# Kernel optimization log

Hardware: AMD Instinct MI355X
Metric: run time of the kernel (lower is better)

## Reference

```python
import jax, jax.numpy as jnp
import numpy as np
from jax import lax

N_ITERS = 3
NUM_CAPS_IN = 768   # 32 * 4 * 6
NUM_CAPS_OUT = 64
CAPS_DIM_IN = 8
CAPS_DIM_OUT = 16


def _conv2d(x, w, b, stride):
    # x: NCHW, w: OIHW, VALID padding
    y = lax.conv_general_dilated(x, w, (stride, stride), 'VALID',
                                 dimension_numbers=('NCHW', 'OIHW', 'NCHW'))
    return y + b[None, :, None, None]


def _squash(x, axis):
    # norm**2 / (1 + norm**2) * x / norm  (as in the torch source)
    norm = jnp.linalg.norm(x, axis=axis, keepdims=True)
    return (norm ** 2) / (1.0 + norm ** 2) * x / norm


def setup_inputs() -> dict:
    key = jax.random.key(0)
    ks = jax.random.split(key, 4)
    B = 128
    x = jax.random.normal(ks[0], (B, 3, 32, 42), dtype=jnp.float32)
    conv1_w = jax.random.normal(ks[1], (32, 3, 6, 6), dtype=jnp.float32) * 0.1
    conv1_b = jnp.zeros((32,), dtype=jnp.float32)
    pc_w = jax.random.normal(ks[2], (256, 32, 3, 3), dtype=jnp.float32) * 0.1
    pc_b = jnp.zeros((256,), dtype=jnp.float32)
    # FinalCapsule W: (num_caps_in, num_caps_out, caps_dim_out, caps_dim_in)
    route_w = jax.random.normal(ks[3], (NUM_CAPS_IN, NUM_CAPS_OUT, CAPS_DIM_OUT, CAPS_DIM_IN), dtype=jnp.float32)
    return {"x": x, "conv1_w": conv1_w, "conv1_b": conv1_b,
            "pc_w": pc_w, "pc_b": pc_b, "route_w": route_w}


def reference(x, conv1_w, conv1_b, pc_w, pc_b, route_w):
    B = x.shape[0]
    # conv1: k=6, s=3 -> (B,32,9,13)
    h = jax.nn.relu(_conv2d(x, conv1_w, conv1_b, 3))
    # primary capsules: k=3, s=2 -> (B,256,4,6) -> (B,768,8)
    h = _conv2d(h, pc_w, pc_b, 2)
    u = h.reshape(B, -1, CAPS_DIM_IN)
    u = _squash(u, axis=-1)
    # prediction vectors: W[i,o,:,:] @ u[b,i,:] -> xh (B, 768, 64, 16)
    xh = jnp.einsum('iokd,bid->biok', route_w, u)
    xhd = lax.stop_gradient(xh)
    b_logits = jnp.zeros((B, NUM_CAPS_IN, NUM_CAPS_OUT), dtype=xh.dtype)
    for _ in range(N_ITERS - 1):
        c = jax.nn.softmax(b_logits, axis=2)                      # (B,768,64)
        s = jnp.sum(c[..., None] * xhd, axis=1, keepdims=True)   # (B,1,64,16)
        v = _squash(s, axis=-1)
        b_logits = b_logits + jnp.sum(xhd * v, axis=-1)
    c = jax.nn.softmax(b_logits, axis=2)
    s = jnp.sum(c[..., None] * xh, axis=1, keepdims=True)
    v = _squash(s, axis=-1)                                       # (B,1,64,16)
    return v[:, 0].reshape(B, NUM_CAPS_OUT * CAPS_DIM_OUT)        # (B,1024)
```

## Files before the change

### kernel.cpp

```cpp
#include <hip/hip_runtime.h>
#include <math.h>

#define BATCH 128
#define NCI 768
#define NCO 64
#define DIN 8
#define DOUT 16

typedef __attribute__((ext_vector_type(8))) short bfrag;
typedef __attribute__((ext_vector_type(4))) float f32x4;
typedef __attribute__((ext_vector_type(16))) float f32x16;

__device__ __forceinline__ void split8(const float* x, bfrag& hi, bfrag& lo) {
    #pragma unroll
    for (int j = 0; j < 8; ++j) {
        unsigned xb = __float_as_uint(x[j]);
        unsigned hb = xb & 0xffff0000u;
        float lf = x[j] - __uint_as_float(hb);
        hi[j] = (short)(xb >> 16);
        lo[j] = (short)(__float_as_uint(lf) >> 16);
    }
}

__global__ __launch_bounds__(256) void conv1_kernel(
    const float* __restrict__ x, const float* __restrict__ w,
    const float* __restrict__ bias, float* __restrict__ h1) {
    __shared__ float wl[32 * 3 * 36];
    for (int i = threadIdx.x; i < 3456; i += 256) wl[i] = w[i];
    __syncthreads();
    int idx = blockIdx.x * 256 + threadIdx.x;
    const int total = BATCH * 32 * 9 * 13;
    if (idx >= total) return;
    int ow = idx % 13; int t = idx / 13;
    int oh = t % 9; t /= 9;
    int oc = t % 32; int b = t / 32;
    float acc = bias[oc];
    const float* xb = x + (size_t)b * 3 * 32 * 42;
    #pragma unroll
    for (int ic = 0; ic < 3; ++ic) {
        const float* xc = xb + ic * 32 * 42 + (oh * 3) * 42 + ow * 3;
        const float* wc = wl + (oc * 3 + ic) * 36;
        #pragma unroll
        for (int kh = 0; kh < 6; ++kh)
            #pragma unroll
            for (int kw = 0; kw < 6; ++kw)
                acc += xc[kh * 42 + kw] * wc[kh * 6 + kw];
    }
    h1[idx] = fmaxf(acc, 0.f);
}

__global__ __launch_bounds__(256) void im2col_kernel(
    const float* __restrict__ h1, float* __restrict__ B2) {
    int idx = blockIdx.x * 256 + threadIdx.x;
    if (idx >= 36 * 3072) return;
    int n = idx % 3072, ko = idx / 3072;
    int b = n / 24, s = n % 24, h = s / 6, w = s % 6;
    const float* hb = h1 + (size_t)b * 3744 + (2 * h) * 13 + 2 * w;
    float out[8];
    #pragma unroll
    for (int j = 0; j < 8; ++j) {
        int k = ko * 8 + j;
        int ic = k / 9, r = k % 9;
        int kh = r / 3, kw = r % 3;
        out[j] = hb[ic * 117 + kh * 13 + kw];
    }
    *(float4*)(B2 + (size_t)idx * 8) = *(const float4*)out;
    *(float4*)(B2 + (size_t)idx * 8 + 4) = *(const float4*)(out + 4);
}

__global__ __launch_bounds__(256) void pc_gemm_kernel(
    const float* __restrict__ wpc, const float* __restrict__ bias,
    const float* __restrict__ B2, float* __restrict__ u2) {
    int wv = threadIdx.x >> 6;
    int l = threadIdx.x & 63;
    int q = l >> 4, r16 = l & 15;
    int c2t = blockIdx.y * 4 + wv;
    int n0 = blockIdx.x * 16;
    f32x4 acc = {0.f, 0.f, 0.f, 0.f};
    int c2a = c2t * 16 + r16;
    const float* ap0 = wpc + (size_t)c2a * 288 + q * 8;
    const float* bp0 = B2 + ((size_t)q * 3072 + n0 + r16) * 8;
    #pragma unroll
    for (int ks = 0; ks < 9; ++ks) {
        float av[8], bv[8];
        *(float4*)av = *(const float4*)(ap0 + ks * 32);
        *(float4*)(av + 4) = *(const float4*)(ap0 + ks * 32 + 4);
        *(float4*)bv = *(const float4*)(bp0 + (size_t)ks * 4 * 3072 * 8);
        *(float4*)(bv + 4) = *(const float4*)(bp0 + (size_t)ks * 4 * 3072 * 8 + 4);
        bfrag ahi, alo, bhi, blo;
        split8(av, ahi, alo);
        split8(bv, bhi, blo);
        acc = __builtin_amdgcn_mfma_f32_16x16x32_bf16(ahi, bhi, acc, 0, 0, 0);
        acc = __builtin_amdgcn_mfma_f32_16x16x32_bf16(ahi, blo, acc, 0, 0, 0);
        acc = __builtin_amdgcn_mfma_f32_16x16x32_bf16(alo, bhi, acc, 0, 0, 0);
    }
    int n = n0 + r16;
    int b = n / 24, s = n % 24;
    float vals[4], n2[4];
    #pragma unroll
    for (int r = 0; r < 4; ++r) {
        float xv = acc[r] + bias[c2t * 16 + q * 4 + r];
        vals[r] = xv;
        n2[r] = xv * xv;
    }
    #pragma unroll
    for (int r = 0; r < 4; ++r) {
        n2[r] += __shfl_xor(n2[r], 1, 64);
        n2[r] += __shfl_xor(n2[r], 2, 64);
        n2[r] += __shfl_xor(n2[r], 4, 64);
    }
    #pragma unroll
    for (int r = 0; r < 4; ++r) {
        int c2 = c2t * 16 + q * 4 + r;
        int cap = c2 * 3 + (s >> 3);
        int d = s & 7;
        float nr = sqrtf(n2[r]);
        u2[((size_t)(cap * 2 + (d >> 2)) * 128 + b) * 4 + (d & 3)]
            = vals[r] * nr / (1.f + n2[r]);
    }
}

__global__ __launch_bounds__(128) void mz_kernel(
    const float* __restrict__ blog, float* __restrict__ m_, float* __restrict__ z_) {
    int i = blockIdx.x;
    int b = threadIdx.x;
    const float* src = blog + (size_t)i * 128 + b;
    float r[64];
    float m = -1e30f;
    #pragma unroll
    for (int o = 0; o < 64; ++o) {
        r[o] = src[(size_t)o * 98304];
        m = fmaxf(m, r[o]);
    }
    float sum = 0.f;
    #pragma unroll
    for (int o = 0; o < 64; ++o) sum += __expf(r[o] - m);
    m_[i * 128 + b] = m;
    z_[i * 128 + b] = 1.f / sum;
}

template <bool UNIFORM>
__global__ __launch_bounds__(256, 4) void spass_kernel(
    const float* __restrict__ W, const float* __restrict__ u2,
    const float* __restrict__ blog, const float* __restrict__ m_,
    const float* __restrict__ z_, float* __restrict__ s_part) {
    int o = blockIdx.x;
    int it = blockIdx.y;
    int tid = threadIdx.x;
    int wv = tid >> 6;
    int l = tid & 63;
    int q = l >> 4, r16 = l & 15;
    int i0 = it * 32;
    __shared__ float wl[32 * 132];

    float4 ua[3][2][2];
    float bl[3][2], mv[3][2], zv[3][2];
    auto issue = [&](int s, int buf) {
        int cap = i0 + s * 4 + q;
        #pragma unroll
        for (int m = 0; m < 2; ++m) {
            int b = wv * 32 + m * 16 + r16;
            ua[buf][m][0] = *(const float4*)(u2 + ((size_t)(cap * 2 + 0) * 128 + b) * 4);
            ua[buf][m][1] = *(const float4*)(u2 + ((size_t)(cap * 2 + 1) * 128 + b) * 4);
            if (!UNIFORM) {
                bl[buf][m] = blog[((size_t)o * 768 + cap) * 128 + b];
                mv[buf][m] = m_[cap * 128 + b];
                zv[buf][m] = z_[cap * 128 + b];
            }
        }
    };

    issue(0, 0);
    issue(1, 1);
    #pragma unroll
    for (int itr = 0; itr < 4; ++itr) {
        int F = tid + 256 * itr;
        int cap = F >> 5, slot = F & 31;
        float4 t4 = *(const float4*)(W + ((size_t)(i0 + cap) * 64 + o) * 128 + slot * 4);
        *(float4*)(wl + cap * 132 + slot * 4) = t4;
    }
    __syncthreads();

    f32x4 acc0 = {0.f, 0.f, 0.f, 0.f};
    f32x4 acc1 = {0.f, 0.f, 0.f, 0.f};
    #pragma unroll
    for (int s = 0; s < 8; ++s) {
        int cur = s % 3;
        if (s < 6) issue(s + 2, (s + 2) % 3);
        const float* wp = wl + (s * 4 + q) * 132 + r16 * 8;
        float wv8[8];
        *(float4*)(wv8) = *(const float4*)wp;
        *(float4*)(wv8 + 4) = *(const float4*)(wp + 4);
        bfrag bhi, blo;
        split8(wv8, bhi, blo);
        #pragma unroll
        for (int m = 0; m < 2; ++m) {
            float uv[8];
            *(float4*)(uv) = ua[cur][m][0];
            *(float4*)(uv + 4) = ua[cur][m][1];
            if (!UNIFORM) {
                float c = __expf(bl[cur][m] - mv[cur][m]) * zv[cur][m];
                #pragma unroll
                for (int j = 0; j < 8; ++j) uv[j] *= c;
            }
            bfrag ahi, alo;
            split8(uv, ahi, alo);
            if (m == 0) {
                acc0 = __builtin_amdgcn_mfma_f32_16x16x32_bf16(ahi, bhi, acc0, 0, 0, 0);
                acc0 = __builtin_amdgcn_mfma_f32_16x16x32_bf16(ahi, blo, acc0, 0, 0, 0);
                acc0 = __builtin_amdgcn_mfma_f32_16x16x32_bf16(alo, bhi, acc0, 0, 0, 0);
            } else {
                acc1 = __builtin_amdgcn_mfma_f32_16x16x32_bf16(ahi, bhi, acc1, 0, 0, 0);
                acc1 = __builtin_amdgcn_mfma_f32_16x16x32_bf16(ahi, blo, acc1, 0, 0, 0);
                acc1 = __builtin_amdgcn_mfma_f32_16x16x32_bf16(alo, bhi, acc1, 0, 0, 0);
            }
        }
    }
    #pragma unroll
    for (int reg = 0; reg < 4; ++reg) {
        int b0 = wv * 32 + q * 4 + reg;
        s_part[(((size_t)it * 128 + b0) * 64 + o) * 16 + r16] = acc0[reg];
        int b1 = b0 + 16;
        s_part[(((size_t)it * 128 + b1) * 64 + o) * 16 + r16] = acc1[reg];
    }
}

template <bool TRANSPOSED>
__global__ __launch_bounds__(256) void squashv_kernel(
    const float* __restrict__ s_part, float* __restrict__ v, float scale) {
    int idx = blockIdx.x * 256 + threadIdx.x;
    float acc = 0.f;
    #pragma unroll
    for (int it = 0; it < 24; ++it) acc += s_part[(size_t)it * 131072 + idx];
    acc *= scale;
    float n2 = acc * acc;
    n2 += __shfl_xor(n2, 1, 64);
    n2 += __shfl_xor(n2, 2, 64);
    n2 += __shfl_xor(n2, 4, 64);
    n2 += __shfl_xor(n2, 8, 64);
    float n = sqrtf(n2);
    float val = acc * n / (1.f + n2);
    if (TRANSPOSED) {
        int k = idx & 15, o = (idx >> 4) & 63, b = idx >> 10;
        v[((size_t)o * 128 + b) * 16 + k] = val;
    } else {
        v[idx] = val;
    }
}

template <bool ACCUM>
__global__ __launch_bounds__(256, 4) void bpass_kernel(
    const float* __restrict__ W, const float* __restrict__ u2,
    const float* __restrict__ v_t, float* __restrict__ blog) {
    int o = blockIdx.x, it = blockIdx.y;
    int tid = threadIdx.x;
    int wv = tid >> 6;
    int l = tid & 63;
    int r = l & 31;
    int kh = l >> 5;
    int capB = it * 32;
    __shared__ float wl[32 * 164];
    #pragma unroll
    for (int itr = 0; itr < 4; ++itr) {
        int F = tid + 256 * itr;
        int cap = F >> 5, slot = F & 31;
        int k = slot >> 1, dh = slot & 1;
        float4 t4 = *(const float4*)(W + ((size_t)(capB + cap) * 64 + o) * 128 + k * 8 + dh * 4);
        float* dst = wl + cap * 164 + (dh * 4) * 20 + k;
        dst[0] = t4.x; dst[20] = t4.y; dst[40] = t4.z; dst[60] = t4.w;
    }
    bfrag vhi[4], vlo[4];
    #pragma unroll
    for (int nt = 0; nt < 4; ++nt) {
        const float* vp = v_t + ((size_t)o * 128 + nt * 32 + r) * 16 + kh * 8;
        float vv8[8];
        *(float4*)(vv8) = *(const float4*)vp;
        *(float4*)(vv8 + 4) = *(const float4*)(vp + 4);
        split8(vv8, vhi[nt], vlo[nt]);
    }
    __syncthreads();
    #pragma unroll
    for (int mt = 0; mt < 2; ++mt) {
        int cl = wv * 8 + mt * 4 + (r >> 3);
        const float* ap = wl + cl * 164 + (r & 7) * 20 + kh * 8;
        float a8[8];
        *(float4*)(a8) = *(const float4*)ap;
        *(float4*)(a8 + 4) = *(const float4*)(ap + 4);
        int capg = capB + wv * 8 + mt * 4;
        int gw = kh * 2;
        float prevv[4][2];
        if (ACCUM) {
            #pragma unroll
            for (int nt = 0; nt < 4; ++nt) {
                int b = nt * 32 + r;
                #pragma unroll
                for (int gg = 0; gg < 2; ++gg)
                    prevv[nt][gg] = blog[((size_t)o * 768 + capg + gw + gg) * 128 + b];
            }
        }
        float4 u4b[2][4];
        #pragma unroll
        for (int g = 0; g < 4; ++g)
            u4b[0][g] = *(const float4*)(u2 + ((size_t)((capg + g) * 2 + kh) * 128 + r) * 4);
        bfrag ahi, alo;
        split8(a8, ahi, alo);
        #pragma unroll
        for (int nt = 0; nt < 4; ++nt) {
            int cur = nt & 1;
            if (nt < 3) {
                int bn = (nt + 1) * 32 + r;
                #pragma unroll
                for (int g = 0; g < 4; ++g)
                    u4b[cur ^ 1][g] = *(const float4*)(u2 + ((size_t)((capg + g) * 2 + kh) * 128 + bn) * 4);
            }
            int b = nt * 32 + r;
            f32x16 acc;
            #pragma unroll
            for (int z = 0; z < 16; ++z) acc[z] = 0.f;
            acc = __builtin_amdgcn_mfma_f32_32x32x16_bf16(ahi, vhi[nt], acc, 0, 0, 0);
            acc = __builtin_amdgcn_mfma_f32_32x32x16_bf16(ahi, vlo[nt], acc, 0, 0, 0);
            acc = __builtin_amdgcn_mfma_f32_32x32x16_bf16(alo, vhi[nt], acc, 0, 0, 0);
            float full[4];
            #pragma unroll
            for (int g = 0; g < 4; ++g) {
                float part = u4b[cur][g].x * acc[g * 4 + 0] + u4b[cur][g].y * acc[g * 4 + 1]
                           + u4b[cur][g].z * acc[g * 4 + 2] + u4b[cur][g].w * acc[g * 4 + 3];
                full[g] = part + __shfl_xor(part, 32, 64);
            }
            #pragma unroll
            for (int gg = 0; gg < 2; ++gg) {
                int g = gw + gg;
                size_t bi = ((size_t)o * 768 + capg + g) * 128 + b;
                blog[bi] = (ACCUM ? prevv[nt][gg] : 0.f) + full[g];
            }
        }
    }
}

extern "C" void kernel_launch(void* const* d_in, const int* in_sizes, int n_in,
                              void* d_out, int out_size, void* d_ws, size_t ws_size,
                              hipStream_t stream) {
    const float* x  = (const float*)d_in[0];
    const float* w1 = (const float*)d_in[1];
    const float* b1 = (const float*)d_in[2];
    const float* wp = (const float*)d_in[3];
    const float* bp = (const float*)d_in[4];
    const float* W  = (const float*)d_in[5];
    float* out = (float*)d_out;
    float* ws = (float*)d_ws;

    float* u2     = ws;
    float* blog   = ws + 786432;
    float* m_     = ws + 7077888;
    float* z_     = ws + 7176192;
    float* v      = ws + 7274496;
    float* s_part = ws + 7405568;
    float* B2     = s_part;
    float* h1     = s_part + 884736;

    conv1_kernel<<<1872, 256, 0, stream>>>(x, w1, b1, h1);
    im2col_kernel<<<432, 256, 0, stream>>>(h1, B2);
    pc_gemm_kernel<<<dim3(192, 4), 256, 0, stream>>>(wp, bp, B2, u2);

    spass_kernel<true><<<dim3(64, 24), 256, 0, stream>>>(W, u2, nullptr, nullptr, nullptr, s_part);
    squashv_kernel<true><<<512, 256, 0, stream>>>(s_part, v, 1.f / 64.f);
    bpass_kernel<false><<<dim3(64, 24), 256, 0, stream>>>(W, u2, v, blog);

    mz_kernel<<<768, 128, 0, stream>>>(blog, m_, z_);
    spass_kernel<false><<<dim3(64, 24), 256, 0, stream>>>(W, u2, blog, m_, z_, s_part);
    squashv_kernel<true><<<512, 256, 0, stream>>>(s_part, v, 1.f);
    bpass_kernel<true><<<dim3(64, 24), 256, 0, stream>>>(W, u2, v, blog);

    mz_kernel<<<768, 128, 0, stream>>>(blog, m_, z_);
    spass_kernel<false><<<dim3(64, 24), 256, 0, stream>>>(W, u2, blog, m_, z_, s_part);
    squashv_kernel<false><<<512, 256, 0, stream>>>(s_part, out, 1.f);
}
```

Before: 160.6 us.

## Fuse conv front end, fold softmax denominator into bpass atomics, drop split-bf16 term

```diff
diff --git a/kernel.cpp b/kernel.cpp
--- a/kernel.cpp
+++ b/kernel.cpp
@@ -1,11 +1,5 @@
 #include <hip/hip_runtime.h>
 #include <math.h>
-
-#define BATCH 128
-#define NCI 768
-#define NCO 64
-#define DIN 8
-#define DOUT 16
 
 typedef __attribute__((ext_vector_type(8))) short bfrag;
 typedef __attribute__((ext_vector_type(4))) float f32x4;
@@ -21,51 +15,58 @@
         lo[j] = (short)(__float_as_uint(lf) >> 16);
     }
 }
-
-__global__ __launch_bounds__(256) void conv1_kernel(
-    const float* __restrict__ x, const float* __restrict__ w,
-    const float* __restrict__ bias, float* __restrict__ h1) {
-    __shared__ float wl[32 * 3 * 36];
-    for (int i = threadIdx.x; i < 3456; i += 256) wl[i] = w[i];
+__device__ __forceinline__ void trunc8(const float* x, bfrag& hi) {
+    #pragma unroll
+    for (int j = 0; j < 8; ++j) hi[j] = (short)(__float_as_uint(x[j]) >> 16);
+}
+
+__global__ __launch_bounds__(256) void front_kernel(
+    const float* __restrict__ x, const float* __restrict__ w1,
+    const float* __restrict__ b1, float* __restrict__ B2) {
+    __shared__ float xl[4032];
+    __shared__ float wl[3456];
+    __shared__ float hl[3744];
+    int b = blockIdx.x, tid = threadIdx.x;
+    const float* xb = x + (size_t)b * 4032;
+    #pragma unroll
+    for (int i = 0; i < 4; ++i) {
+        int idx = tid + 256 * i;
+        if (idx < 1008) *(float4*)(xl + idx * 4) = *(const float4*)(xb + idx * 4);
+        if (idx < 864)  *(float4*)(wl + idx * 4) = *(const float4*)(w1 + idx * 4);
+    }
     __syncthreads();
-    int idx = blockIdx.x * 256 + threadIdx.x;
-    const int total = BATCH * 32 * 9 * 13;
-    if (idx >= total) return;
-    int ow = idx % 13; int t = idx / 13;
-    int oh = t % 9; t /= 9;
-    int oc = t % 32; int b = t / 32;
-    float acc = bias[oc];
-    const float* xb = x + (size_t)b * 3 * 32 * 42;
-    #pragma unroll
-    for (int ic = 0; ic < 3; ++ic) {
-        const float* xc = xb + ic * 32 * 42 + (oh * 3) * 42 + ow * 3;
-        const float* wc = wl + (oc * 3 + ic) * 36;
-        #pragma unroll
-        for (int kh = 0; kh < 6; ++kh)
-            #pragma unroll
-            for (int kw = 0; kw < 6; ++kw)
-                acc += xc[kh * 42 + kw] * wc[kh * 6 + kw];
-    }
-    h1[idx] = fmaxf(acc, 0.f);
-}
-
-__global__ __launch_bounds__(256) void im2col_kernel(
-    const float* __restrict__ h1, float* __restrict__ B2) {
-    int idx = blockIdx.x * 256 + threadIdx.x;
-    if (idx >= 36 * 3072) return;
-    int n = idx % 3072, ko = idx / 3072;
-    int b = n / 24, s = n % 24, h = s / 6, w = s % 6;
-    const float* hb = h1 + (size_t)b * 3744 + (2 * h) * 13 + 2 * w;
-    float out[8];
-    #pragma unroll
-    for (int j = 0; j < 8; ++j) {
-        int k = ko * 8 + j;
-        int ic = k / 9, r = k % 9;
-        int kh = r / 3, kw = r % 3;
-        out[j] = hb[ic * 117 + kh * 13 + kw];
-    }
-    *(float4*)(B2 + (size_t)idx * 8) = *(const float4*)out;
-    *(float4*)(B2 + (size_t)idx * 8 + 4) = *(const float4*)(out + 4);
+    for (int idx = tid; idx < 3744; idx += 256) {
+        int oc = idx / 117, r = idx % 117;
+        int oh = r / 13, ow = r % 13;
+        float acc = b1[oc];
+        #pragma unroll
+        for (int ic = 0; ic < 3; ++ic) {
+            const float* xc = xl + ic * 1344 + (oh * 3) * 42 + ow * 3;
+            const float* wc = wl + (oc * 3 + ic) * 36;
+            #pragma unroll
+            for (int kh = 0; kh < 6; ++kh)
+                #pragma unroll
+                for (int kw = 0; kw < 6; ++kw)
+                    acc += xc[kh * 42 + kw] * wc[kh * 6 + kw];
+        }
+        hl[idx] = fmaxf(acc, 0.f);
+    }
+    __syncthreads();
+    for (int f = tid; f < 864; f += 256) {
+        int ko = f / 24, s = f % 24;
+        int h = s / 6, w = s % 6;
+        float o8[8];
+        #pragma unroll
+        for (int j = 0; j < 8; ++j) {
+            int k = ko * 8 + j;
+            int ic = k / 9, rr = k % 9;
+            int kh = rr / 3, kw = rr % 3;
+            o8[j] = hl[ic * 117 + (2 * h + kh) * 13 + (2 * w + kw)];
+        }
+        float* dst = B2 + ((size_t)ko * 3072 + b * 24 + s) * 8;
+        *(float4*)dst = *(const float4*)o8;
+        *(float4*)(dst + 4) = *(const float4*)(o8 + 4);
+    }
 }
 
 __global__ __launch_bounds__(256) void pc_gemm_kernel(
@@ -77,16 +78,15 @@
     int c2t = blockIdx.y * 4 + wv;
     int n0 = blockIdx.x * 16;
     f32x4 acc = {0.f, 0.f, 0.f, 0.f};
-    int c2a = c2t * 16 + r16;
-    const float* ap0 = wpc + (size_t)c2a * 288 + q * 8;
+    const float* ap0 = wpc + (size_t)(c2t * 16 + r16) * 288 + q * 8;
     const float* bp0 = B2 + ((size_t)q * 3072 + n0 + r16) * 8;
     #pragma unroll
     for (int ks = 0; ks < 9; ++ks) {
         float av[8], bv[8];
         *(float4*)av = *(const float4*)(ap0 + ks * 32);
         *(float4*)(av + 4) = *(const float4*)(ap0 + ks * 32 + 4);
-        *(float4*)bv = *(const float4*)(bp0 + (size_t)ks * 4 * 3072 * 8);
-        *(float4*)(bv + 4) = *(const float4*)(bp0 + (size_t)ks * 4 * 3072 * 8 + 4);
+        *(float4*)bv = *(const float4*)(bp0 + (size_t)ks * 98304);
+        *(float4*)(bv + 4) = *(const float4*)(bp0 + (size_t)ks * 98304 + 4);
         bfrag ahi, alo, bhi, blo;
         split8(av, ahi, alo);
         split8(bv, bhi, blo);
@@ -120,30 +120,11 @@
     }
 }
 
-__global__ __launch_bounds__(128) void mz_kernel(
-    const float* __restrict__ blog, float* __restrict__ m_, float* __restrict__ z_) {
-    int i = blockIdx.x;
-    int b = threadIdx.x;
-    const float* src = blog + (size_t)i * 128 + b;
-    float r[64];
-    float m = -1e30f;
-    #pragma unroll
-    for (int o = 0; o < 64; ++o) {
-        r[o] = src[(size_t)o * 98304];
-        m = fmaxf(m, r[o]);
-    }
-    float sum = 0.f;
-    #pragma unroll
-    for (int o = 0; o < 64; ++o) sum += __expf(r[o] - m);
-    m_[i * 128 + b] = m;
-    z_[i * 128 + b] = 1.f / sum;
-}
-
 template <bool UNIFORM>
 __global__ __launch_bounds__(256, 4) void spass_kernel(
     const float* __restrict__ W, const float* __restrict__ u2,
-    const float* __restrict__ blog, const float* __restrict__ m_,
-    const float* __restrict__ z_, float* __restrict__ s_part) {
+    const float* __restrict__ blog, const float* __restrict__ zsum,
+    float* __restrict__ s_part) {
     int o = blockIdx.x;
     int it = blockIdx.y;
     int tid = threadIdx.x;
@@ -154,7 +135,7 @@
     __shared__ float wl[32 * 132];
 
     float4 ua[3][2][2];
-    float bl[3][2], mv[3][2], zv[3][2];
+    float blv[3][2], zv[3][2];
     auto issue = [&](int s, int buf) {
         int cap = i0 + s * 4 + q;
         #pragma unroll
@@ -163,9 +144,8 @@
             ua[buf][m][0] = *(const float4*)(u2 + ((size_t)(cap * 2 + 0) * 128 + b) * 4);
             ua[buf][m][1] = *(const float4*)(u2 + ((size_t)(cap * 2 + 1) * 128 + b) * 4);
             if (!UNIFORM) {
-                bl[buf][m] = blog[((size_t)o * 768 + cap) * 128 + b];
-                mv[buf][m] = m_[cap * 128 + b];
-                zv[buf][m] = z_[cap * 128 + b];
+                blv[buf][m] = blog[((size_t)o * 768 + cap) * 128 + b];
+                zv[buf][m]  = zsum[cap * 128 + b];
             }
         }
     };
@@ -176,8 +156,8 @@
     for (int itr = 0; itr < 4; ++itr) {
         int F = tid + 256 * itr;
         int cap = F >> 5, slot = F & 31;
-        float4 t4 = *(const float4*)(W + ((size_t)(i0 + cap) * 64 + o) * 128 + slot * 4);
-        *(float4*)(wl + cap * 132 + slot * 4) = t4;
+        *(float4*)(wl + cap * 132 + slot * 4) =
+            *(const float4*)(W + ((size_t)(i0 + cap) * 64 + o) * 128 + slot * 4);
     }
     __syncthreads();
 
@@ -199,20 +179,18 @@
             *(float4*)(uv) = ua[cur][m][0];
             *(float4*)(uv + 4) = ua[cur][m][1];
             if (!UNIFORM) {
-                float c = __expf(bl[cur][m] - mv[cur][m]) * zv[cur][m];
+                float c = __expf(blv[cur][m]) / zv[cur][m];
                 #pragma unroll
                 for (int j = 0; j < 8; ++j) uv[j] *= c;
             }
-            bfrag ahi, alo;
-            split8(uv, ahi, alo);
+            bfrag ahi;
+            trunc8(uv, ahi);
             if (m == 0) {
                 acc0 = __builtin_amdgcn_mfma_f32_16x16x32_bf16(ahi, bhi, acc0, 0, 0, 0);
                 acc0 = __builtin_amdgcn_mfma_f32_16x16x32_bf16(ahi, blo, acc0, 0, 0, 0);
-                acc0 = __builtin_amdgcn_mfma_f32_16x16x32_bf16(alo, bhi, acc0, 0, 0, 0);
             } else {
                 acc1 = __builtin_amdgcn_mfma_f32_16x16x32_bf16(ahi, bhi, acc1, 0, 0, 0);
                 acc1 = __builtin_amdgcn_mfma_f32_16x16x32_bf16(ahi, blo, acc1, 0, 0, 0);
-                acc1 = __builtin_amdgcn_mfma_f32_16x16x32_bf16(alo, bhi, acc1, 0, 0, 0);
             }
         }
     }
@@ -220,8 +198,7 @@
     for (int reg = 0; reg < 4; ++reg) {
         int b0 = wv * 32 + q * 4 + reg;
         s_part[(((size_t)it * 128 + b0) * 64 + o) * 16 + r16] = acc0[reg];
-        int b1 = b0 + 16;
-        s_part[(((size_t)it * 128 + b1) * 64 + o) * 16 + r16] = acc1[reg];
+        s_part[(((size_t)it * 128 + b0 + 16) * 64 + o) * 16 + r16] = acc1[reg];
     }
 }
 
@@ -251,7 +228,8 @@
 template <bool ACCUM>
 __global__ __launch_bounds__(256, 4) void bpass_kernel(
     const float* __restrict__ W, const float* __restrict__ u2,
-    const float* __restrict__ v_t, float* __restrict__ blog) {
+    const float* __restrict__ v_t, float* __restrict__ blog,
+    float* __restrict__ zsum) {
     int o = blockIdx.x, it = blockIdx.y;
     int tid = threadIdx.x;
     int wv = tid >> 6;
@@ -330,8 +308,10 @@
             #pragma unroll
             for (int gg = 0; gg < 2; ++gg) {
                 int g = gw + gg;
-                size_t bi = ((size_t)o * 768 + capg + g) * 128 + b;
-                blog[bi] = (ACCUM ? prevv[nt][gg] : 0.f) + full[g];
+                int cap = capg + g;
+                float nb = (ACCUM ? prevv[nt][gg] : 0.f) + full[g];
+                blog[((size_t)o * 768 + cap) * 128 + b] = nb;
+                atomicAdd(zsum + cap * 128 + b, __expf(nb));
             }
         }
     }
@@ -351,27 +331,24 @@
 
     float* u2     = ws;
     float* blog   = ws + 786432;
-    float* m_     = ws + 7077888;
-    float* z_     = ws + 7176192;
+    float* zsum   = ws + 7077888;
     float* v      = ws + 7274496;
     float* s_part = ws + 7405568;
     float* B2     = s_part;
-    float* h1     = s_part + 884736;
-
-    conv1_kernel<<<1872, 256, 0, stream>>>(x, w1, b1, h1);
-    im2col_kernel<<<432, 256, 0, stream>>>(h1, B2);
+
+    front_kernel<<<128, 256, 0, stream>>>(x, w1, b1, B2);
     pc_gemm_kernel<<<dim3(192, 4), 256, 0, stream>>>(wp, bp, B2, u2);
 
-    spass_kernel<true><<<dim3(64, 24), 256, 0, stream>>>(W, u2, nullptr, nullptr, nullptr, s_part);
+    spass_kernel<true><<<dim3(64, 24), 256, 0, stream>>>(W, u2, nullptr, nullptr, s_part);
     squashv_kernel<true><<<512, 256, 0, stream>>>(s_part, v, 1.f / 64.f);
-    bpass_kernel<false><<<dim3(64, 24), 256, 0, stream>>>(W, u2, v, blog);
-
-    mz_kernel<<<768, 128, 0, stream>>>(blog, m_, z_);
-    spass_kernel<false><<<dim3(64, 24), 256, 0, stream>>>(W, u2, blog, m_, z_, s_part);
+    hipMemsetAsync(zsum, 0, 98304 * sizeof(float), stream);
+    bpass_kernel<false><<<dim3(64, 24), 256, 0, stream>>>(W, u2, v, blog, zsum);
+
+    spass_kernel<false><<<dim3(64, 24), 256, 0, stream>>>(W, u2, blog, zsum, s_part);
     squashv_kernel<true><<<512, 256, 0, stream>>>(s_part, v, 1.f);
-    bpass_kernel<true><<<dim3(64, 24), 256, 0, stream>>>(W, u2, v, blog);
-
-    mz_kernel<<<768, 128, 0, stream>>>(blog, m_, z_);
-    spass_kernel<false><<<dim3(64, 24), 256, 0, stream>>>(W, u2, blog, m_, z_, s_part);
+    hipMemsetAsync(zsum, 0, 98304 * sizeof(float), stream);
+    bpass_kernel<true><<<dim3(64, 24), 256, 0, stream>>>(W, u2, v, blog, zsum);
+
+    spass_kernel<false><<<dim3(64, 24), 256, 0, stream>>>(W, u2, blog, zsum, s_part);
     squashv_kernel<false><<<512, 256, 0, stream>>>(s_part, out, 1.f);
 }
```

Result: slower. 174.8 us (+8.8%).
